# Performance work log

Measured on AMD Instinct MI355X. Metric: run time of the kernel, lower is better.

Reference implementation:

```python
import jax, jax.numpy as jnp
import numpy as np

E_ROUTER = 32      # routed experts with real FFNs
ZERO_E = 8         # zero-experts (identity skip)
TOP_K = 4
ROUTED_SCALE = 2.5


def setup_inputs() -> dict:
    key = jax.random.key(0)
    k1, k2, k3, k4, k5 = jax.random.split(key, 5)
    T, H, I = 2048, 1024, 512
    N = E_ROUTER + ZERO_E
    return {
        "hidden_states": jax.random.normal(k1, (T, H), jnp.float32),
        "router_w": jax.random.normal(k2, (N, H), jnp.float32) * 0.02,            # classifier weight [N, H]
        "e_score_correction_bias": jax.random.normal(k3, (N,), jnp.float32) * 0.01,
        "w13": jax.random.normal(k4, (E_ROUTER, 2 * I, H), jnp.float32) * 0.02,   # gate+up per expert
        "w2": jax.random.normal(k5, (E_ROUTER, H, I), jnp.float32) * 0.02,        # down proj per expert
    }


def reference(hidden_states, router_w, e_score_correction_bias, w13, w2):
    T, H = hidden_states.shape
    I = w2.shape[-1]

    # --- router (LongcatFlashTopkRouter) ---
    logits = hidden_states @ router_w.T                         # [T, N]
    scores = jax.nn.softmax(logits, axis=-1)
    biased = scores + e_score_correction_bias[None, :]
    _, topk_ids = jax.lax.top_k(biased, TOP_K)                  # indices chosen on biased scores
    topk_w = jnp.take_along_axis(scores, topk_ids, axis=-1) * ROUTED_SCALE  # weights from unbiased scores

    # --- zero experts: ids >= E_ROUTER contribute weight * x directly ---
    zero_mask = topk_ids >= E_ROUTER
    zero_total = jnp.sum(jnp.where(zero_mask, topk_w, 0.0), axis=-1, keepdims=True)  # [T,1]
    zero_expert_output = hidden_states * zero_total
    topk_w = jnp.where(zero_mask, 0.0, topk_w)
    topk_ids = jnp.where(zero_mask, 0, topk_ids)

    # --- combine weights per (token, expert): scatter-add of topk weights ---
    combine = jnp.zeros((T, E_ROUTER), jnp.float32).at[
        jnp.arange(T)[:, None], topk_ids
    ].add(topk_w)                                               # [T, E]

    # --- experts: swiglu FFN per expert (dense form of grouped GEMM; zero combine
    #     weights make it mathematically identical to dispatch/compute/combine) ---
    gate_up = jnp.einsum('th,eih->eti', hidden_states, w13)     # [E, T, 2I]
    gate, up = gate_up[..., :I], gate_up[..., I:]
    h = jax.nn.silu(gate) * up                                  # [E, T, I]
    expert_out = jnp.einsum('eti,ehi->eth', h, w2)              # [E, T, H]
    routed = jnp.einsum('eth,te->th', expert_out, combine)      # [T, H]

    return routed + zero_expert_output
```

## Files before the change

### kernel.cpp

```cpp
#include <hip/hip_runtime.h>
#include <math.h>

#define TT 2048
#define HH 1024
#define NE 40
#define ER 32
#define II 512
#define TOPK 4
#define RSCALE 2.5f
#define MAXW 64

typedef __bf16 bf16x8 __attribute__((ext_vector_type(8)));
typedef float f32x4 __attribute__((ext_vector_type(4)));

__global__ __launch_bounds__(256) void k_router(const float* __restrict__ hidden,
                                                const float* __restrict__ rw,
                                                const float* __restrict__ bias,
                                                float* __restrict__ out,
                                                int* __restrict__ tok4_id,
                                                float* __restrict__ tok4_w,
                                                __bf16* __restrict__ hid_bf) {
  int lane = threadIdx.x & 63;
  int t = blockIdx.x * 4 + (threadIdx.x >> 6);
  const float* hrow = hidden + (size_t)t * HH;
  float4 hv[4];
  #pragma unroll
  for (int c = 0; c < 4; c++) hv[c] = *(const float4*)(hrow + c * 256 + lane * 4);

  float mylg = -INFINITY;
  for (int e = 0; e < NE; e++) {
    const float* wrow = rw + (size_t)e * HH;
    float p = 0.f;
    #pragma unroll
    for (int c = 0; c < 4; c++) {
      float4 w4 = *(const float4*)(wrow + c * 256 + lane * 4);
      p += hv[c].x * w4.x + hv[c].y * w4.y + hv[c].z * w4.z + hv[c].w * w4.w;
    }
    #pragma unroll
    for (int off = 32; off; off >>= 1) p += __shfl_xor(p, off);
    if (lane == e) mylg = p;
  }
  float m = mylg;
  #pragma unroll
  for (int off = 32; off; off >>= 1) m = fmaxf(m, __shfl_xor(m, off));
  float p = (lane < NE) ? expf(mylg - m) : 0.f;
  float s = p;
  #pragma unroll
  for (int off = 32; off; off >>= 1) s += __shfl_xor(s, off);
  float score = p / s;
  float v = (lane < NE) ? score + bias[lane] : -INFINITY;
  int ids[TOPK]; float wv[TOPK];
  #pragma unroll
  for (int k = 0; k < TOPK; k++) {
    float mv = v;
    int mi = (lane < NE) ? lane : 63;
    #pragma unroll
    for (int off = 32; off; off >>= 1) {
      float ov = __shfl_xor(mv, off);
      int oi = __shfl_xor(mi, off);
      if (ov > mv || (ov == mv && oi < mi)) { mv = ov; mi = oi; }
    }
    ids[k] = mi;
    wv[k] = RSCALE * __shfl(score, mi);
    if (lane == mi) v = -INFINITY;
  }
  float zt = 0.f;
  #pragma unroll
  for (int k = 0; k < TOPK; k++) if (ids[k] >= ER) zt += wv[k];
  if (lane == 0) {
    #pragma unroll
    for (int k = 0; k < TOPK; k++) {
      tok4_id[t * TOPK + k] = ids[k];
      tok4_w[t * TOPK + k] = wv[k];
    }
  }
  #pragma unroll
  for (int c = 0; c < 4; c++) {
    int j = c * 256 + lane * 4;
    float4 h4 = hv[c];
    *(float4*)(out + (size_t)t * HH + j) =
        make_float4(h4.x * zt, h4.y * zt, h4.z * zt, h4.w * zt);
    union { __bf16 h[4]; uint2 u; } pk;
    pk.h[0] = (__bf16)h4.x; pk.h[1] = (__bf16)h4.y;
    pk.h[2] = (__bf16)h4.z; pk.h[3] = (__bf16)h4.w;
    *(uint2*)(hid_bf + (size_t)t * HH + j) = pk.u;
  }
}

__global__ __launch_bounds__(256) void k_scanscatter(const int* __restrict__ tok4_id,
                                                     const float* __restrict__ tok4_w,
                                                     int* __restrict__ cnt,
                                                     int* __restrict__ offs,
                                                     int* __restrict__ wl_e,
                                                     int* __restrict__ wl_m0,
                                                     int* __restrict__ nwork,
                                                     int* __restrict__ pair_tok,
                                                     float* __restrict__ pair_w) {
  __shared__ int scnt[32];
  __shared__ int scur[32];
  int tid = threadIdx.x;
  if (tid < 32) scnt[tid] = 0;
  __syncthreads();
  int ids[32]; float wv[32];
  #pragma unroll
  for (int i = 0; i < 32; i++) {
    int idx = i * 256 + tid;
    ids[i] = tok4_id[idx];
    wv[i] = tok4_w[idx];
    if (ids[i] < ER) atomicAdd(&scnt[ids[i]], 1);
  }
  __syncthreads();
  if (tid < 64) {
    int lane = tid;
    int c = (lane < ER) ? scnt[lane] : 0;
    int ts = (c + 255) >> 8;
    int ps = c, pt = ts;
    #pragma unroll
    for (int off = 1; off < 32; off <<= 1) {
      int v1 = __shfl_up(ps, off);
      int v2 = __shfl_up(pt, off);
      if (lane >= off) { ps += v1; pt += v2; }
    }
    if (lane < ER) {
      int o = ps - c;
      offs[lane] = o; cnt[lane] = c; scur[lane] = o;
      int tb = pt - ts;
      for (int i = 0; i < ts; i++) { wl_e[tb + i] = lane; wl_m0[tb + i] = i * 256; }
    }
    if (lane == 31) *nwork = pt;
  }
  __syncthreads();
  #pragma unroll
  for (int i = 0; i < 32; i++) {
    if (ids[i] < ER) {
      int pos = atomicAdd(&scur[ids[i]], 1);
      pair_tok[pos] = (i * 256 + tid) >> 2;
      pair_w[pos] = wv[i];
    }
  }
}

__global__ __launch_bounds__(256) void k_w13(const __bf16* __restrict__ hid_bf,
                                             const float* __restrict__ w13,
                                             const int* __restrict__ cnt,
                                             const int* __restrict__ offs,
                                             const int* __restrict__ pair_tok,
                                             const int* __restrict__ wl_e,
                                             const int* __restrict__ wl_m0,
                                             const int* __restrict__ nwork,
                                             __bf16* __restrict__ h_buf) {
  int bx = blockIdx.x;
  if (bx >= *nwork) return;
  int e = wl_e[bx], m0w = wl_m0[bx];
  int M = cnt[e] - m0w; if (M > 256) M = 256;
  int base = offs[e] + m0w;
  int n0 = blockIdx.y * 32;

  __shared__ __bf16 As[256][72];
  __shared__ __bf16 Bs[64][72];
  __shared__ int tl[256];

  int tid = threadIdx.x;
  int lane = tid & 63, w = tid >> 6;
  int quad = lane >> 4, rr = lane & 15;

  tl[tid] = pair_tok[base + ((tid < M) ? tid : 0)];

  const float* wg_base = w13 + (size_t)e * (2 * II) * HH + (size_t)n0 * HH;
  const float* wu_base = w13 + (size_t)e * (2 * II) * HH + (size_t)(II + n0) * HH;

  f32x4 accg[4][2] = {};
  f32x4 accu[4][2] = {};
  __syncthreads();

  for (int k0 = 0; k0 < HH; k0 += 64) {
    #pragma unroll
    for (int p = 0; p < 8; p++) {
      int s = p * 256 + tid;
      int r = s >> 3, c = (s & 7) * 8;
      *(uint4*)&As[r][c] = *(const uint4*)(hid_bf + (size_t)tl[r] * HH + k0 + c);
    }
    #pragma unroll
    for (int p = 0; p < 4; p++) {
      int s = p * 256 + tid;
      int r = s >> 4, c = (s & 15) * 4;
      const float* src = ((r < 32) ? (wg_base + (size_t)r * HH)
                                   : (wu_base + (size_t)(r - 32) * HH)) + k0 + c;
      float4 v = *(const float4*)src;
      union { __bf16 h[4]; uint2 u; } pk;
      pk.h[0] = (__bf16)v.x; pk.h[1] = (__bf16)v.y;
      pk.h[2] = (__bf16)v.z; pk.h[3] = (__bf16)v.w;
      *(uint2*)&Bs[r][c] = pk.u;
    }
    __syncthreads();
    #pragma unroll
    for (int ks = 0; ks < 2; ks++) {
      int kb = ks * 32 + quad * 8;
      bf16x8 a[4], bg[2], bu[2];
      #pragma unroll
      for (int i = 0; i < 4; i++) a[i] = *(const bf16x8*)&As[w * 64 + i * 16 + rr][kb];
      #pragma unroll
      for (int j = 0; j < 2; j++) {
        bg[j] = *(const bf16x8*)&Bs[j * 16 + rr][kb];
        bu[j] = *(const bf16x8*)&Bs[32 + j * 16 + rr][kb];
      }
      #pragma unroll
      for (int i = 0; i < 4; i++)
        #pragma unroll
        for (int j = 0; j < 2; j++) {
          accg[i][j] = __builtin_amdgcn_mfma_f32_16x16x32_bf16(a[i], bg[j], accg[i][j], 0, 0, 0);
          accu[i][j] = __builtin_amdgcn_mfma_f32_16x16x32_bf16(a[i], bu[j], accu[i][j], 0, 0, 0);
        }
    }
    __syncthreads();
  }
  #pragma unroll
  for (int i = 0; i < 4; i++)
    #pragma unroll
    for (int j = 0; j < 2; j++)
      #pragma unroll
      for (int l = 0; l < 4; l++) {
        int m = w * 64 + i * 16 + quad * 4 + l;
        if (m < M) {
          float g = accg[i][j][l], u = accu[i][j][l];
          float hv = g / (1.f + expf(-g)) * u;
          h_buf[(size_t)(base + m) * II + n0 + j * 16 + rr] = (__bf16)hv;
        }
      }
}

__global__ __launch_bounds__(256) void k_w2(const __bf16* __restrict__ h_buf,
                                            const float* __restrict__ w2,
                                            const int* __restrict__ cnt,
                                            const int* __restrict__ offs,
                                            const int* __restrict__ pair_tok,
                                            const float* __restrict__ pair_w,
                                            const int* __restrict__ wl_e,
                                            const int* __restrict__ wl_m0,
                                            const int* __restrict__ nwork,
                                            float* __restrict__ out) {
  int bx = blockIdx.x;
  if (bx >= *nwork) return;
  int e = wl_e[bx], m0w = wl_m0[bx];
  int M = cnt[e] - m0w; if (M > 256) M = 256;
  int base = offs[e] + m0w;
  int h0 = blockIdx.y * 64;

  __shared__ __bf16 As[256][72];
  __shared__ __bf16 Bs[64][72];
  __shared__ int tl[256];
  __shared__ float wl[256];

  int tid = threadIdx.x;
  int lane = tid & 63, w = tid >> 6;
  int quad = lane >> 4, rr = lane & 15;

  {
    int ok = tid < M;
    tl[tid] = ok ? pair_tok[base + tid] : 0;
    wl[tid] = ok ? pair_w[base + tid] : 0.f;
  }
  const __bf16* h_base = h_buf + (size_t)base * II;
  const float* w_base = w2 + (size_t)e * HH * II + (size_t)h0 * II;

  f32x4 acc[4][4] = {};
  __syncthreads();

  for (int k0 = 0; k0 < II; k0 += 64) {
    #pragma unroll
    for (int p = 0; p < 8; p++) {
      int s = p * 256 + tid;
      int r = s >> 3, c = (s & 7) * 8;
      *(uint4*)&As[r][c] = *(const uint4*)(h_base + (size_t)r * II + k0 + c);
    }
    #pragma unroll
    for (int p = 0; p < 4; p++) {
      int s = p * 256 + tid;
      int r = s >> 4, c = (s & 15) * 4;
      float4 v = *(const float4*)(w_base + (size_t)r * II + k0 + c);
      union { __bf16 h[4]; uint2 u; } pk;
      pk.h[0] = (__bf16)v.x; pk.h[1] = (__bf16)v.y;
      pk.h[2] = (__bf16)v.z; pk.h[3] = (__bf16)v.w;
      *(uint2*)&Bs[r][c] = pk.u;
    }
    __syncthreads();
    #pragma unroll
    for (int ks = 0; ks < 2; ks++) {
      int kb = ks * 32 + quad * 8;
      bf16x8 a[4], b[4];
      #pragma unroll
      for (int i = 0; i < 4; i++) a[i] = *(const bf16x8*)&As[w * 64 + i * 16 + rr][kb];
      #pragma unroll
      for (int j = 0; j < 4; j++) b[j] = *(const bf16x8*)&Bs[j * 16 + rr][kb];
      #pragma unroll
      for (int i = 0; i < 4; i++)
        #pragma unroll
        for (int j = 0; j < 4; j++)
          acc[i][j] = __builtin_amdgcn_mfma_f32_16x16x32_bf16(a[i], b[j], acc[i][j], 0, 0, 0);
    }
    __syncthreads();
  }
  #pragma unroll
  for (int i = 0; i < 4; i++)
    #pragma unroll
    for (int l = 0; l < 4; l++) {
      int m = w * 64 + i * 16 + quad * 4 + l;
      if (m < M) {
        int t = tl[m];
        float wp = wl[m];
        #pragma unroll
        for (int j = 0; j < 4; j++)
          atomicAdd(&out[(size_t)t * HH + h0 + j * 16 + rr], acc[i][j][l] * wp);
      }
    }
}

extern "C" void kernel_launch(void* const* d_in, const int* in_sizes, int n_in,
                              void* d_out, int out_size, void* d_ws, size_t ws_size,
                              hipStream_t stream) {
  const float* hidden = (const float*)d_in[0];
  const float* rw     = (const float*)d_in[1];
  const float* bias   = (const float*)d_in[2];
  const float* w13    = (const float*)d_in[3];
  const float* w2     = (const float*)d_in[4];
  float* out = (float*)d_out;

  int* ws_i = (int*)d_ws;
  int* tok4_id = ws_i;
  float* tok4_w = (float*)(tok4_id + TT * TOPK);
  int* pair_tok = (int*)(tok4_w + TT * TOPK);
  float* pair_w = (float*)(pair_tok + TT * TOPK);
  int* cnt = (int*)(pair_w + TT * TOPK);
  int* offs = cnt + 32;
  int* wl_e = offs + 32;
  int* wl_m0 = wl_e + 64;
  int* nwork = wl_m0 + 64;
  __bf16* hid_bf = (__bf16*)(nwork + 64);
  __bf16* h_buf = hid_bf + (size_t)TT * HH;

  k_router<<<dim3(TT / 4), dim3(256), 0, stream>>>(hidden, rw, bias, out,
                                                   tok4_id, tok4_w, hid_bf);
  k_scanscatter<<<dim3(1), dim3(256), 0, stream>>>(tok4_id, tok4_w, cnt, offs,
                                                   wl_e, wl_m0, nwork, pair_tok, pair_w);
  k_w13<<<dim3(MAXW, 16), dim3(256), 0, stream>>>(hid_bf, w13, cnt, offs, pair_tok,
                                                  wl_e, wl_m0, nwork, h_buf);
  k_w2<<<dim3(MAXW, 16), dim3(256), 0, stream>>>(h_buf, w2, cnt, offs, pair_tok, pair_w,
                                                 wl_e, wl_m0, nwork, out);
}
```

Measured before the change: 340.8 us.

## Drop LDS staging in expert GEMMs, load MFMA fragments directly from global

Both expert GEMM kernels (gate/up and down projection) stop staging A and B tiles through shared memory with barriers. Each lane now loads its MFMA operand fragments straight from global memory, converting fp32 weights to bf16 in registers. This removes the LDS write/read traffic and the __syncthreads stalls. In exchange, each of the four waves now fetches the same weight fragments separately, and the gathered activation rows come in as uncoalesced 16-byte reads, which relies on the cache to absorb the redundancy.

```diff
diff --git a/kernel.cpp b/kernel.cpp
--- a/kernel.cpp
+++ b/kernel.cpp
@@ -12,6 +12,13 @@
 
 typedef __bf16 bf16x8 __attribute__((ext_vector_type(8)));
 typedef float f32x4 __attribute__((ext_vector_type(4)));
+
+__device__ __forceinline__ bf16x8 cvt_bf8(float4 lo, float4 hi) {
+  bf16x8 r;
+  r[0] = (__bf16)lo.x; r[1] = (__bf16)lo.y; r[2] = (__bf16)lo.z; r[3] = (__bf16)lo.w;
+  r[4] = (__bf16)hi.x; r[5] = (__bf16)hi.y; r[6] = (__bf16)hi.z; r[7] = (__bf16)hi.w;
+  return r;
+}
 
 __global__ __launch_bounds__(256) void k_router(const float* __restrict__ hidden,
                                                 const float* __restrict__ rw,
@@ -156,63 +163,56 @@
   int base = offs[e] + m0w;
   int n0 = blockIdx.y * 32;
 
-  __shared__ __bf16 As[256][72];
-  __shared__ __bf16 Bs[64][72];
   __shared__ int tl[256];
-
   int tid = threadIdx.x;
   int lane = tid & 63, w = tid >> 6;
   int quad = lane >> 4, rr = lane & 15;
 
   tl[tid] = pair_tok[base + ((tid < M) ? tid : 0)];
-
-  const float* wg_base = w13 + (size_t)e * (2 * II) * HH + (size_t)n0 * HH;
-  const float* wu_base = w13 + (size_t)e * (2 * II) * HH + (size_t)(II + n0) * HH;
+  __syncthreads();
+
+  const __bf16* ap[4];
+  #pragma unroll
+  for (int i = 0; i < 4; i++)
+    ap[i] = hid_bf + (size_t)tl[w * 64 + i * 16 + rr] * HH + quad * 8;
+
+  const float* wbase = w13 + (size_t)e * (2 * II) * HH;
+  const float* bgp[2];
+  const float* bup[2];
+  #pragma unroll
+  for (int j = 0; j < 2; j++) {
+    bgp[j] = wbase + (size_t)(n0 + j * 16 + rr) * HH + quad * 8;
+    bup[j] = wbase + (size_t)(II + n0 + j * 16 + rr) * HH + quad * 8;
+  }
 
   f32x4 accg[4][2] = {};
   f32x4 accu[4][2] = {};
-  __syncthreads();
-
-  for (int k0 = 0; k0 < HH; k0 += 64) {
-    #pragma unroll
-    for (int p = 0; p < 8; p++) {
-      int s = p * 256 + tid;
-      int r = s >> 3, c = (s & 7) * 8;
-      *(uint4*)&As[r][c] = *(const uint4*)(hid_bf + (size_t)tl[r] * HH + k0 + c);
-    }
-    #pragma unroll
-    for (int p = 0; p < 4; p++) {
-      int s = p * 256 + tid;
-      int r = s >> 4, c = (s & 15) * 4;
-      const float* src = ((r < 32) ? (wg_base + (size_t)r * HH)
-                                   : (wu_base + (size_t)(r - 32) * HH)) + k0 + c;
-      float4 v = *(const float4*)src;
-      union { __bf16 h[4]; uint2 u; } pk;
-      pk.h[0] = (__bf16)v.x; pk.h[1] = (__bf16)v.y;
-      pk.h[2] = (__bf16)v.z; pk.h[3] = (__bf16)v.w;
-      *(uint2*)&Bs[r][c] = pk.u;
-    }
-    __syncthreads();
-    #pragma unroll
-    for (int ks = 0; ks < 2; ks++) {
-      int kb = ks * 32 + quad * 8;
-      bf16x8 a[4], bg[2], bu[2];
-      #pragma unroll
-      for (int i = 0; i < 4; i++) a[i] = *(const bf16x8*)&As[w * 64 + i * 16 + rr][kb];
+
+  #pragma unroll 2
+  for (int k0 = 0; k0 < HH; k0 += 32) {
+    bf16x8 a[4];
+    #pragma unroll
+    for (int i = 0; i < 4; i++) a[i] = *(const bf16x8*)(ap[i] + k0);
+    bf16x8 bg[2], bu[2];
+    #pragma unroll
+    for (int j = 0; j < 2; j++) {
+      float4 lo = *(const float4*)(bgp[j] + k0);
+      float4 hi = *(const float4*)(bgp[j] + k0 + 4);
+      bg[j] = cvt_bf8(lo, hi);
+    }
+    #pragma unroll
+    for (int j = 0; j < 2; j++) {
+      float4 lo = *(const float4*)(bup[j] + k0);
+      float4 hi = *(const float4*)(bup[j] + k0 + 4);
+      bu[j] = cvt_bf8(lo, hi);
+    }
+    #pragma unroll
+    for (int i = 0; i < 4; i++)
       #pragma unroll
       for (int j = 0; j < 2; j++) {
-        bg[j] = *(const bf16x8*)&Bs[j * 16 + rr][kb];
-        bu[j] = *(const bf16x8*)&Bs[32 + j * 16 + rr][kb];
+        accg[i][j] = __builtin_amdgcn_mfma_f32_16x16x32_bf16(a[i], bg[j], accg[i][j], 0, 0, 0);
+        accu[i][j] = __builtin_amdgcn_mfma_f32_16x16x32_bf16(a[i], bu[j], accu[i][j], 0, 0, 0);
       }
-      #pragma unroll
-      for (int i = 0; i < 4; i++)
-        #pragma unroll
-        for (int j = 0; j < 2; j++) {
-          accg[i][j] = __builtin_amdgcn_mfma_f32_16x16x32_bf16(a[i], bg[j], accg[i][j], 0, 0, 0);
-          accu[i][j] = __builtin_amdgcn_mfma_f32_16x16x32_bf16(a[i], bu[j], accu[i][j], 0, 0, 0);
-        }
-    }
-    __syncthreads();
   }
   #pragma unroll
   for (int i = 0; i < 4; i++)
@@ -246,8 +246,6 @@
   int base = offs[e] + m0w;
   int h0 = blockIdx.y * 64;
 
-  __shared__ __bf16 As[256][72];
-  __shared__ __bf16 Bs[64][72];
   __shared__ int tl[256];
   __shared__ float wl[256];
 
@@ -260,45 +258,38 @@
     tl[tid] = ok ? pair_tok[base + tid] : 0;
     wl[tid] = ok ? pair_w[base + tid] : 0.f;
   }
-  const __bf16* h_base = h_buf + (size_t)base * II;
-  const float* w_base = w2 + (size_t)e * HH * II + (size_t)h0 * II;
+  __syncthreads();
+
+  const __bf16* ap[4];
+  #pragma unroll
+  for (int i = 0; i < 4; i++)
+    ap[i] = h_buf + (size_t)(base + w * 64 + i * 16 + rr) * II + quad * 8;
+
+  const float* w_base = w2 + (size_t)e * HH * II;
+  const float* bp[4];
+  #pragma unroll
+  for (int j = 0; j < 4; j++)
+    bp[j] = w_base + (size_t)(h0 + j * 16 + rr) * II + quad * 8;
 
   f32x4 acc[4][4] = {};
-  __syncthreads();
-
-  for (int k0 = 0; k0 < II; k0 += 64) {
-    #pragma unroll
-    for (int p = 0; p < 8; p++) {
-      int s = p * 256 + tid;
-      int r = s >> 3, c = (s & 7) * 8;
-      *(uint4*)&As[r][c] = *(const uint4*)(h_base + (size_t)r * II + k0 + c);
-    }
-    #pragma unroll
-    for (int p = 0; p < 4; p++) {
-      int s = p * 256 + tid;
-      int r = s >> 4, c = (s & 15) * 4;
-      float4 v = *(const float4*)(w_base + (size_t)r * II + k0 + c);
-      union { __bf16 h[4]; uint2 u; } pk;
-      pk.h[0] = (__bf16)v.x; pk.h[1] = (__bf16)v.y;
-      pk.h[2] = (__bf16)v.z; pk.h[3] = (__bf16)v.w;
-      *(uint2*)&Bs[r][c] = pk.u;
-    }
-    __syncthreads();
-    #pragma unroll
-    for (int ks = 0; ks < 2; ks++) {
-      int kb = ks * 32 + quad * 8;
-      bf16x8 a[4], b[4];
+
+  #pragma unroll 2
+  for (int k0 = 0; k0 < II; k0 += 32) {
+    bf16x8 a[4];
+    #pragma unroll
+    for (int i = 0; i < 4; i++) a[i] = *(const bf16x8*)(ap[i] + k0);
+    bf16x8 b[4];
+    #pragma unroll
+    for (int j = 0; j < 4; j++) {
+      float4 lo = *(const float4*)(bp[j] + k0);
+      float4 hi = *(const float4*)(bp[j] + k0 + 4);
+      b[j] = cvt_bf8(lo, hi);
+    }
+    #pragma unroll
+    for (int i = 0; i < 4; i++)
       #pragma unroll
-      for (int i = 0; i < 4; i++) a[i] = *(const bf16x8*)&As[w * 64 + i * 16 + rr][kb];
-      #pragma unroll
-      for (int j = 0; j < 4; j++) b[j] = *(const bf16x8*)&Bs[j * 16 + rr][kb];
-      #pragma unroll
-      for (int i = 0; i < 4; i++)
-        #pragma unroll
-        for (int j = 0; j < 4; j++)
-          acc[i][j] = __builtin_amdgcn_mfma_f32_16x16x32_bf16(a[i], b[j], acc[i][j], 0, 0, 0);
-    }
-    __syncthreads();
+      for (int j = 0; j < 4; j++)
+        acc[i][j] = __builtin_amdgcn_mfma_f32_16x16x32_bf16(a[i], b[j], acc[i][j], 0, 0, 0);
   }
   #pragma unroll
   for (int i = 0; i < 4; i++)
```

After: 487.5 us. 1.43x slower.
